# Kernel optimization log

Measured on AMD Instinct MI355X. Metric: run time of the kernel, lower is better.

The kernel has to match this reference:

```python
import jax, jax.numpy as jnp
import numpy as np

D_MODEL = 1024
NUM_HEADS = 16
DK = D_MODEL // NUM_HEADS


def setup_inputs() -> dict:
    key = jax.random.key(0)
    ks = jax.random.split(key, 12)
    B, S, D = 2, 2048, D_MODEL
    s = 1.0 / np.sqrt(D)
    inp = {
        "Q": jax.random.normal(ks[0], (B, S, D), jnp.float32),
        "K": jax.random.normal(ks[1], (B, S, D), jnp.float32),
        "V": jax.random.normal(ks[2], (B, S, D), jnp.float32),
        "Wq": jax.random.uniform(ks[3], (D, D), jnp.float32, -s, s),
        "bq": jax.random.uniform(ks[4], (D,), jnp.float32, -s, s),
        "Wk": jax.random.uniform(ks[5], (D, D), jnp.float32, -s, s),
        "bk": jax.random.uniform(ks[6], (D,), jnp.float32, -s, s),
        "Wv": jax.random.uniform(ks[7], (D, D), jnp.float32, -s, s),
        "bv": jax.random.uniform(ks[8], (D,), jnp.float32, -s, s),
        "Wo": jax.random.uniform(ks[9], (D, D), jnp.float32, -s, s),
        "bo": jax.random.uniform(ks[10], (D,), jnp.float32, -s, s),
    }
    return inp


def reference(Q, K, V, Wq, bq, Wk, bk, Wv, bv, Wo, bo):
    B, S, D = Q.shape
    H, dk = NUM_HEADS, DK
    # projections (torch Linear: x @ W.T + b), split heads -> [B,H,S,dk]
    q = (Q @ Wq.T + bq).reshape(B, S, H, dk).transpose(0, 2, 1, 3)
    k = (K @ Wk.T + bk).reshape(B, S, H, dk).transpose(0, 2, 1, 3)
    v = (V @ Wv.T + bv).reshape(B, S, H, dk).transpose(0, 2, 1, 3)
    scores = jnp.einsum("bhqd,bhkd->bhqk", q, k) / jnp.sqrt(jnp.asarray(dk, q.dtype))
    attn = jax.nn.softmax(scores, axis=-1)
    out = jnp.einsum("bhqk,bhkd->bhqd", attn, v)  # [B,H,S,dk]
    out = out.transpose(0, 2, 1, 3).reshape(B, S, D)
    return out @ Wo.T + bo
```

## Files before the change

### kernel.cpp

```cpp
#include <hip/hip_runtime.h>
#include <stdint.h>


#define AS1 __attribute__((address_space(1)))
#define AS3 __attribute__((address_space(3)))

typedef unsigned short u16;
typedef short s16x8 __attribute__((ext_vector_type(8)));
typedef float f32x4 __attribute__((ext_vector_type(4)));
typedef float f32x16 __attribute__((ext_vector_type(16)));
typedef u16   u16x4 __attribute__((ext_vector_type(4)));

#if defined(__has_builtin)
#if __has_builtin(__builtin_amdgcn_exp2f)
#define EXP2F(x) __builtin_amdgcn_exp2f(x)
#else
#define EXP2F(x) exp2f(x)
#endif
#else
#define EXP2F(x) exp2f(x)
#endif

__device__ __forceinline__ u16 f2b(float f) {
  union { float f; uint32_t u; } v;
  v.f = f;
  uint32_t r = (v.u + 0x7fffu + ((v.u >> 16) & 1u)) >> 16;
  return (u16)r;
}

__device__ __forceinline__ uint32_t cvtpk(float lo, float hi) {
  uint32_t r;
  asm("v_cvt_pk_bf16_f32 %0, %1, %2" : "=v"(r) : "v"(lo), "v"(hi));
  return r;
}

__device__ __forceinline__ float max3f(float a, float b, float c) {
  float r;
  asm("v_max3_f32 %0, %1, %2, %3" : "=v"(r) : "v"(a), "v"(b), "v"(c));
  return r;
}

__device__ __forceinline__ f32x4 mfma16(s16x8 a, s16x8 b, f32x4 c) {
  return __builtin_amdgcn_mfma_f32_16x16x32_bf16(a, b, c, 0, 0, 0);
}

__device__ __forceinline__ f32x16 mfma32(s16x8 a, s16x8 b, f32x16 c) {
  return __builtin_amdgcn_mfma_f32_32x32x16_bf16(a, b, c, 0, 0, 0);
}

__device__ __forceinline__ s16x8 ld_g16(const u16* p) {
  return *reinterpret_cast<const s16x8*>(p);
}

__device__ __forceinline__ void stage16(const u16* g, u16* lds_base) {
  __builtin_amdgcn_global_load_lds((const AS1 unsigned int*)g,
                                   (AS3 unsigned int*)lds_base, 16, 0, 0);
}

struct CvtArgs {
  const float* src[7];
  u16* dst[7];
  int cum[8];
};

__global__ __launch_bounds__(256) void cvt_all(CvtArgs a) {
  const int bx = blockIdx.x;
  int seg = 0;
#pragma unroll
  for (int i = 1; i < 7; ++i) seg += (bx >= a.cum[i]) ? 1 : 0;
  const int off = (bx - a.cum[seg]) * 256 + threadIdx.x;
  float4 f = reinterpret_cast<const float4*>(a.src[seg])[off];
  union { u16 u[4]; uint64_t q; } o;
  o.u[0] = f2b(f.x); o.u[1] = f2b(f.y); o.u[2] = f2b(f.z); o.u[3] = f2b(f.w);
  reinterpret_cast<uint64_t*>(a.dst[seg])[off] = o.q;
}

template <int MODE>
__global__ __launch_bounds__(256) void gemm_bt(const u16* __restrict__ Abase,
                                               const u16* __restrict__ Wbase,
                                               const float* __restrict__ bias0,
                                               const float* __restrict__ bias1,
                                               const float* __restrict__ bias2,
                                               u16* __restrict__ outb,
                                               u16* __restrict__ vtout,
                                               float* __restrict__ outf) {
  __shared__ u16 As[2][128 * 64];
  __shared__ u16 Bs[2][128 * 64];
  const int tid = threadIdx.x;
  const int lane = tid & 63;
  const int w = tid >> 6;
  const int wr = w >> 1, wc = w & 1;

  const int bid = blockIdx.y * 8 + blockIdx.x;
  const int sw = (bid & 7) * 32 + (bid >> 3);
  const int n0 = (sw & 7) * 128;
  const int m0 = (sw >> 3) * 128;
  const int z = (MODE == 0) ? blockIdx.z : 0;
  const float QSC = 0.18033688011112042f;

  const u16* A = Abase + (size_t)z * (4096u * 1024u);
  const u16* W = Wbase + (size_t)z * (1024u * 1024u);
  const float* bias = (MODE == 0) ? (z == 0 ? bias0 : (z == 1 ? bias1 : bias2)) : bias0;
  u16* ob = (MODE == 0) ? (outb + (size_t)z * (4096u * 1024u)) : nullptr;

  const int l15 = lane & 15, l4 = lane >> 4;

  const int sr = lane >> 3;
  const int sx = lane & 7;
  const u16* gA[4];
  const u16* gB[4];
#pragma unroll
  for (int j = 0; j < 4; ++j) {
    const int row = w * 32 + j * 8 + sr;
    const int lc = ((sx ^ (row & 7)) << 3);
    gA[j] = A + (size_t)(m0 + row) * 1024 + lc;
    gB[j] = W + (size_t)(n0 + row) * 1024 + lc;
  }

  f32x4 acc[4][4];
#pragma unroll
  for (int i = 0; i < 4; ++i)
#pragma unroll
    for (int j = 0; j < 4; ++j) acc[i][j] = {0.f, 0.f, 0.f, 0.f};

#pragma unroll
  for (int j = 0; j < 4; ++j) {
    stage16(gA[j], &As[0][(w * 32 + j * 8) * 64]);
    stage16(gB[j], &Bs[0][(w * 32 + j * 8) * 64]);
  }
  __syncthreads();

#pragma unroll 2
  for (int t = 0; t < 16; ++t) {
    const int cur = t & 1;
    if (t + 1 < 16) {
      const int kt = (t + 1) * 64;
#pragma unroll
      for (int j = 0; j < 4; ++j) {
        stage16(gA[j] + kt, &As[cur ^ 1][(w * 32 + j * 8) * 64]);
        stage16(gB[j] + kt, &Bs[cur ^ 1][(w * 32 + j * 8) * 64]);
      }
    }
#pragma unroll
    for (int ks = 0; ks < 2; ++ks) {
      s16x8 af[4], bf[4];
#pragma unroll
      for (int mi = 0; mi < 4; ++mi) {
        const int row = wr * 64 + mi * 16 + l15;
        const int sc_ = (((ks << 2) | l4) ^ (l15 & 7)) << 3;
        af[mi] = *(const s16x8*)&As[cur][row * 64 + sc_];
      }
#pragma unroll
      for (int ni = 0; ni < 4; ++ni) {
        const int row = wc * 64 + ni * 16 + l15;
        const int sc_ = (((ks << 2) | l4) ^ (l15 & 7)) << 3;
        bf[ni] = *(const s16x8*)&Bs[cur][row * 64 + sc_];
      }
      __builtin_amdgcn_s_setprio(1);
#pragma unroll
      for (int mi = 0; mi < 4; ++mi)
#pragma unroll
        for (int ni = 0; ni < 4; ++ni)
          acc[mi][ni] = mfma16(af[mi], bf[ni], acc[mi][ni]);
      __builtin_amdgcn_s_setprio(0);
    }
    __syncthreads();
  }

#pragma unroll
  for (int ni = 0; ni < 4; ++ni) {
    const int col = n0 + wc * 64 + ni * 16 + l15;
    const float bv = bias[col];
#pragma unroll
    for (int mi = 0; mi < 4; ++mi) {
      const int row0 = m0 + wr * 64 + mi * 16 + l4 * 4;
      if (MODE == 0 && z == 2) {
        const int b = row0 >> 11, s0 = row0 & 2047;
        const int pos0 = (s0 & ~15) | ((s0 & 4) << 1) | ((s0 & 8) >> 1);
        const int h = col >> 6, d = col & 63;
        u16x4 pk = {f2b(acc[mi][ni][0] + bv), f2b(acc[mi][ni][1] + bv),
                    f2b(acc[mi][ni][2] + bv), f2b(acc[mi][ni][3] + bv)};
        *(u16x4*)&vtout[((size_t)(b * 16 + h) * 64 + d) * 2048 + pos0] = pk;
      } else {
#pragma unroll
        for (int r = 0; r < 4; ++r) {
          float val = acc[mi][ni][r] + bv;
          const int row = row0 + r;
          if (MODE == 0) {
            if (z == 0) val *= QSC;
            const int b = row >> 11, s = row & 2047;
            const int h = col >> 6, d = col & 63;
            ob[((size_t)(b * 16 + h) * 2048 + s) * 64 + d] = f2b(val);
          } else {
            outf[(size_t)row * 1024 + col] = val;
          }
        }
      }
    }
  }
}

__global__ __launch_bounds__(512, 2) void fattn(const u16* __restrict__ qp,
                                                const u16* __restrict__ kp,
                                                const u16* __restrict__ vt,
                                                u16* __restrict__ ao) {
  __shared__ u16 Kt[2][4096];
  __shared__ u16 Vt[2][4096];

  const int lane = threadIdx.x & 63;
  const int w = threadIdx.x >> 6;
  const int bh = blockIdx.y;
  const int b = bh >> 4, h = bh & 15;
  const int q0 = blockIdx.x * 256 + w * 32;
  const u16* qb = qp + (size_t)bh * (2048 * 64);
  const u16* kb = kp + (size_t)bh * (2048 * 64);
  const u16* vb = vt + (size_t)bh * (64 * 2048);
  const int l31 = lane & 31, hl = lane >> 5;
  const int x7 = l31 & 7;
  const float THR = 8.0f;

  const int srow = (w << 3) + (lane >> 3);
  const int c0 = (((lane & 7) ^ (srow & 7)) << 3);

  s16x8 qa[4];
#pragma unroll
  for (int kc = 0; kc < 4; ++kc)
    qa[kc] = ld_g16(qb + (size_t)(q0 + l31) * 64 + kc * 16 + hl * 8);

  f32x16 o[2];
  float lsum = 0.f;
  float mrun = 0.f;
#pragma unroll
  for (int r = 0; r < 16; ++r) { o[0][r] = 0.f; o[1][r] = 0.f; }

  stage16(kb + (size_t)srow * 64 + c0, &Kt[0][w * 512]);
  stage16(vb + (size_t)srow * 2048 + c0, &Vt[0][w * 512]);
  __syncthreads();

#pragma unroll 2
  for (int t = 0; t < 32; ++t) {
    const int cur = t & 1;
    if (t + 1 < 32) {
      const int kk = (t + 1) << 6;
      stage16(kb + (size_t)(kk + srow) * 64 + c0, &Kt[cur ^ 1][w * 512]);
      stage16(vb + (size_t)srow * 2048 + kk + c0, &Vt[cur ^ 1][w * 512]);
    }

    f32x16 sc[2];
#pragma unroll
    for (int r = 0; r < 16; ++r) { sc[0][r] = -mrun; sc[1][r] = -mrun; }
#pragma unroll
    for (int nk = 0; nk < 2; ++nk) {
      s16x8 kf[4];
#pragma unroll
      for (int kc = 0; kc < 4; ++kc)
        kf[kc] = *(const s16x8*)&Kt[cur][(nk * 32 + l31) * 64 +
                                         ((((kc << 1) | hl) ^ x7) << 3)];
      __builtin_amdgcn_s_setprio(1);
#pragma unroll
      for (int kc = 0; kc < 4; ++kc)
        sc[nk] = mfma32(kf[kc], qa[kc], sc[nk]);
      __builtin_amdgcn_s_setprio(0);
    }

    float m = -1e30f;
#pragma unroll
    for (int nk = 0; nk < 2; ++nk)
#pragma unroll
      for (int r = 0; r < 16; r += 2)
        m = max3f(m, sc[nk][r], sc[nk][r + 1]);
    m = fmaxf(m, __shfl_xor(m, 32));

    if (__any(m > THR)) {
      const float d = fmaxf(m, 0.f);
      mrun += d;
      const float alpha = EXP2F(-d);
      lsum *= alpha;
#pragma unroll
      for (int r = 0; r < 16; ++r) { sc[0][r] -= d; sc[1][r] -= d; }
#pragma unroll
      for (int r = 0; r < 16; ++r) {
        float ar = __shfl(alpha, (r & 3) + 8 * (r >> 2) + 4 * hl);
        o[0][r] *= ar; o[1][r] *= ar;
      }
    }

#pragma unroll
    for (int nk = 0; nk < 2; ++nk) {
      float p[16];
#pragma unroll
      for (int r = 0; r < 16; ++r) p[r] = EXP2F(sc[nk][r]);
#pragma unroll
      for (int r = 0; r < 16; ++r) lsum += p[r];
#pragma unroll
      for (int kc = 0; kc < 2; ++kc) {
        union { uint32_t d[4]; s16x8 v; } pa;
        pa.d[0] = cvtpk(p[kc * 8 + 0], p[kc * 8 + 1]);
        pa.d[1] = cvtpk(p[kc * 8 + 2], p[kc * 8 + 3]);
        pa.d[2] = cvtpk(p[kc * 8 + 4], p[kc * 8 + 5]);
        pa.d[3] = cvtpk(p[kc * 8 + 6], p[kc * 8 + 7]);
        const int chunk = nk * 4 + kc * 2 + hl;
#pragma unroll
        for (int dt = 0; dt < 2; ++dt) {
          s16x8 vf = *(const s16x8*)&Vt[cur][(dt * 32 + l31) * 64 +
                                             ((chunk ^ x7) << 3)];
          __builtin_amdgcn_s_setprio(1);
          o[dt] = mfma32(pa.v, vf, o[dt]);
          __builtin_amdgcn_s_setprio(0);
        }
      }
    }

    __syncthreads();
  }

  lsum += __shfl_xor(lsum, 32);
#pragma unroll
  for (int r = 0; r < 16; ++r) {
    const int qreg = (r & 3) + 8 * (r >> 2) + 4 * hl;
    const float inv = 1.0f / __shfl(lsum, qreg);
    const int row = b * 2048 + q0 + qreg;
#pragma unroll
    for (int dt = 0; dt < 2; ++dt)
      ao[(size_t)row * 1024 + h * 64 + dt * 32 + l31] = f2b(o[dt][r] * inv);
  }
}

extern "C" void kernel_launch(void* const* d_in, const int* in_sizes, int n_in,
                              void* d_out, int out_size, void* d_ws, size_t ws_size,
                              hipStream_t stream) {
  const float* Q  = (const float*)d_in[0];
  const float* K  = (const float*)d_in[1];
  const float* V  = (const float*)d_in[2];
  const float* Wq = (const float*)d_in[3];
  const float* bq = (const float*)d_in[4];
  const float* Wk = (const float*)d_in[5];
  const float* bk = (const float*)d_in[6];
  const float* Wv = (const float*)d_in[7];
  const float* bv = (const float*)d_in[8];
  const float* Wo = (const float*)d_in[9];
  const float* bo = (const float*)d_in[10];
  float* out = (float*)d_out;

  const size_t NI = (size_t)4096 * 1024;
  const size_t NW = (size_t)1024 * 1024;
  u16* XB  = (u16*)d_ws;
  u16* WB  = XB + 3 * NI;
  u16* QKV = WB + 4 * NW;
  u16* VT  = QKV + 3 * NI;
  u16* AO  = VT + NI;

  CvtArgs ca;
  ca.src[0] = Q;  ca.dst[0] = XB;
  ca.src[1] = K;  ca.dst[1] = XB + NI;
  ca.src[2] = V;  ca.dst[2] = XB + 2 * NI;
  ca.src[3] = Wq; ca.dst[3] = WB;
  ca.src[4] = Wk; ca.dst[4] = WB + NW;
  ca.src[5] = Wv; ca.dst[5] = WB + 2 * NW;
  ca.src[6] = Wo; ca.dst[6] = WB + 3 * NW;
  ca.cum[0] = 0;     ca.cum[1] = 4096;  ca.cum[2] = 8192;  ca.cum[3] = 12288;
  ca.cum[4] = 13312; ca.cum[5] = 14336; ca.cum[6] = 15360; ca.cum[7] = 16384;
  cvt_all<<<dim3(16384), 256, 0, stream>>>(ca);

  gemm_bt<0><<<dim3(8, 32, 3), 256, 0, stream>>>(XB, WB, bq, bk, bv, QKV, VT, nullptr);
  fattn<<<dim3(8, 32), 512, 0, stream>>>(QKV, QKV + NI, VT, AO);
  gemm_bt<1><<<dim3(8, 32, 1), 256, 0, stream>>>(AO, WB + 3 * NW, bo, nullptr, nullptr,
                                                 nullptr, nullptr, out);
}
```

Baseline: 128.0 us.

## Software-pipeline attention: overlap next tile's QK^T with softmax/PV using triple-buffered LDS

Restructures the flash-attention kernel so the QK^T MFMAs for the next key tile are issued while the current tile's softmax and PV run. It adds a third LDS buffer rotated between staging, QK and PV roles, with a lagged running-max correction. Blocks shrink from 8 waves to 4 waves and 128 queries, and the grid doubles to keep the same coverage. This is meant to hide MFMA and LDS latency behind exp work, at the cost of more registers for the two score sets and more LDS per block.

Measured after the change: 133.2 us. +4.1%, slower.

```diff
diff --git a/kernel.cpp b/kernel.cpp
--- a/kernel.cpp
+++ b/kernel.cpp
@@ -200,18 +200,20 @@
   }
 }
 
-__global__ __launch_bounds__(512, 2) void fattn(const u16* __restrict__ qp,
+__global__ __launch_bounds__(256, 2) void fattn(const u16* __restrict__ qp,
                                                 const u16* __restrict__ kp,
                                                 const u16* __restrict__ vt,
                                                 u16* __restrict__ ao) {
-  __shared__ u16 Kt[2][4096];
-  __shared__ u16 Vt[2][4096];
+  __shared__ u16 Kt[3][4096];
+  __shared__ u16 Vt[3][4096];
+  u16* Ksh = &Kt[0][0];
+  u16* Vsh = &Vt[0][0];
 
   const int lane = threadIdx.x & 63;
   const int w = threadIdx.x >> 6;
   const int bh = blockIdx.y;
   const int b = bh >> 4, h = bh & 15;
-  const int q0 = blockIdx.x * 256 + w * 32;
+  const int q0 = blockIdx.x * 128 + w * 32;
   const u16* qb = qp + (size_t)bh * (2048 * 64);
   const u16* kb = kp + (size_t)bh * (2048 * 64);
   const u16* vb = vt + (size_t)bh * (64 * 2048);
@@ -219,100 +221,131 @@
   const int x7 = l31 & 7;
   const float THR = 8.0f;
 
-  const int srow = (w << 3) + (lane >> 3);
-  const int c0 = (((lane & 7) ^ (srow & 7)) << 3);
+  const int srow = (w << 4) + (lane >> 3);
+  const int c0 = (((lane & 7) ^ (lane >> 3)) << 3);
+
+#define STAGE(kk, bo)                                                          \
+  do {                                                                         \
+    stage16(kb + (size_t)((kk) + srow) * 64 + c0, Ksh + (bo) + w * 1024);      \
+    stage16(kb + (size_t)((kk) + srow + 8) * 64 + c0, Ksh + (bo) + w * 1024 + 512); \
+    stage16(vb + (size_t)srow * 2048 + (kk) + c0, Vsh + (bo) + w * 1024);      \
+    stage16(vb + (size_t)(srow + 8) * 2048 + (kk) + c0, Vsh + (bo) + w * 1024 + 512); \
+  } while (0)
 
   s16x8 qa[4];
 #pragma unroll
   for (int kc = 0; kc < 4; ++kc)
     qa[kc] = ld_g16(qb + (size_t)(q0 + l31) * 64 + kc * 16 + hl * 8);
 
-  f32x16 o[2];
+  f32x16 o0, o1;
+  f32x16 scA0, scA1, scB0, scB1;
   float lsum = 0.f;
   float mrun = 0.f;
-#pragma unroll
-  for (int r = 0; r < 16; ++r) { o[0][r] = 0.f; o[1][r] = 0.f; }
-
-  stage16(kb + (size_t)srow * 64 + c0, &Kt[0][w * 512]);
-  stage16(vb + (size_t)srow * 2048 + c0, &Vt[0][w * 512]);
+  float mbA = 0.f, mbB = 0.f;
+#pragma unroll
+  for (int r = 0; r < 16; ++r) { o0[r] = 0.f; o1[r] = 0.f; }
+
+#define QKT(N0, N1, MBN, BO)                                                   \
+  do {                                                                         \
+    MBN = mrun;                                                                \
+    const float ini_ = -mrun;                                                  \
+    _Pragma("unroll") for (int r = 0; r < 16; ++r) { N0[r] = ini_; N1[r] = ini_; } \
+    s16x8 kf0_[4], kf1_[4];                                                    \
+    _Pragma("unroll") for (int kc = 0; kc < 4; ++kc) {                         \
+      kf0_[kc] = *(const s16x8*)&Ksh[(BO) + (0 * 32 + l31) * 64 +              \
+                                     ((((kc << 1) | hl) ^ x7) << 3)];          \
+      kf1_[kc] = *(const s16x8*)&Ksh[(BO) + (1 * 32 + l31) * 64 +              \
+                                     ((((kc << 1) | hl) ^ x7) << 3)];          \
+    }                                                                          \
+    __builtin_amdgcn_s_setprio(1);                                             \
+    _Pragma("unroll") for (int kc = 0; kc < 4; ++kc) N0 = mfma32(kf0_[kc], qa[kc], N0); \
+    _Pragma("unroll") for (int kc = 0; kc < 4; ++kc) N1 = mfma32(kf1_[kc], qa[kc], N1); \
+    __builtin_amdgcn_s_setprio(0);                                             \
+  } while (0)
+
+#define SMPV(S0, S1, MB, BO)                                                   \
+  do {                                                                         \
+    float x1 = max3f(S0[0], S0[1], S0[2]);                                     \
+    float x2 = max3f(S0[3], S0[4], S0[5]);                                     \
+    float x3 = max3f(S0[6], S0[7], S0[8]);                                     \
+    float x4 = max3f(S0[9], S0[10], S0[11]);                                   \
+    float x5 = max3f(S0[12], S0[13], S0[14]);                                  \
+    float x6 = max3f(S0[15], S1[0], S1[1]);                                    \
+    float x7_ = max3f(S1[2], S1[3], S1[4]);                                    \
+    float x8 = max3f(S1[5], S1[6], S1[7]);                                     \
+    float x9 = max3f(S1[8], S1[9], S1[10]);                                    \
+    float xa = max3f(S1[11], S1[12], S1[13]);                                  \
+    float xb = max3f(S1[14], S1[15], x1);                                      \
+    float xc = max3f(x2, x3, x4);                                              \
+    float xd = max3f(x5, x6, x7_);                                             \
+    float xe = max3f(x8, x9, xa);                                              \
+    float mrel = fmaxf(max3f(xb, xc, xd), xe);                                 \
+    mrel = fmaxf(mrel, __shfl_xor(mrel, 32));                                  \
+    float base_ = MB - mrun;                                                   \
+    if (__any(mrel + base_ > THR)) {                  \
+      float d_ = fmaxf(mrel + base_, 0.f);                                     \
+      mrun += d_; base_ -= d_;                                                 \
+      float al_ = EXP2F(-d_);                                                  \
+      lsum *= al_;                                                             \
+      _Pragma("unroll") for (int r = 0; r < 16; ++r) {                         \
+        float ar_ = __shfl(al_, (r & 3) + 8 * (r >> 2) + 4 * hl);              \
+        o0[r] *= ar_; o1[r] *= ar_;                                            \
+      }                                                                        \
+    }                                                                          \
+    if (__any(base_ != 0.f)) {                      \
+      _Pragma("unroll") for (int r = 0; r < 16; ++r) { S0[r] += base_; S1[r] += base_; } \
+    }                                                                          \
+    float p0_[16], p1_[16];                                                    \
+    _Pragma("unroll") for (int r = 0; r < 16; ++r) p0_[r] = EXP2F(S0[r]);      \
+    _Pragma("unroll") for (int r = 0; r < 16; ++r) p1_[r] = EXP2F(S1[r]);      \
+    _Pragma("unroll") for (int r = 0; r < 16; ++r) lsum += p0_[r] + p1_[r];    \
+    _Pragma("unroll") for (int nk = 0; nk < 2; ++nk) {                         \
+      float* pp_ = nk ? p1_ : p0_;                                             \
+      _Pragma("unroll") for (int kc = 0; kc < 2; ++kc) {                       \
+        union { uint32_t d[4]; s16x8 v; } pa_;                                 \
+        pa_.d[0] = cvtpk(pp_[kc * 8 + 0], pp_[kc * 8 + 1]);                    \
+        pa_.d[1] = cvtpk(pp_[kc * 8 + 2], pp_[kc * 8 + 3]);                    \
+        pa_.d[2] = cvtpk(pp_[kc * 8 + 4], pp_[kc * 8 + 5]);                    \
+        pa_.d[3] = cvtpk(pp_[kc * 8 + 6], pp_[kc * 8 + 7]);                    \
+        const int chunk_ = nk * 4 + kc * 2 + hl;                               \
+        s16x8 vf0_ = *(const s16x8*)&Vsh[(BO) + (0 * 32 + l31) * 64 +          \
+                                         ((chunk_ ^ x7) << 3)];                \
+        s16x8 vf1_ = *(const s16x8*)&Vsh[(BO) + (1 * 32 + l31) * 64 +          \
+                                         ((chunk_ ^ x7) << 3)];                \
+        __builtin_amdgcn_s_setprio(1);                                         \
+        o0 = mfma32(pa_.v, vf0_, o0);                                          \
+        o1 = mfma32(pa_.v, vf1_, o1);                                          \
+        __builtin_amdgcn_s_setprio(0);                                         \
+      }                                                                        \
+    }                                                                          \
+  } while (0)
+
+#define ROT()                                                                  \
+  do { const int t_ = b_pv; b_pv = b_qk; b_qk = b_st; b_st = t_; } while (0)
+
+  int b_pv = 0, b_qk = 4096, b_st = 8192;
+
+  STAGE(0, 0);
   __syncthreads();
-
-#pragma unroll 2
-  for (int t = 0; t < 32; ++t) {
-    const int cur = t & 1;
-    if (t + 1 < 32) {
-      const int kk = (t + 1) << 6;
-      stage16(kb + (size_t)(kk + srow) * 64 + c0, &Kt[cur ^ 1][w * 512]);
-      stage16(vb + (size_t)srow * 2048 + kk + c0, &Vt[cur ^ 1][w * 512]);
-    }
-
-    f32x16 sc[2];
-#pragma unroll
-    for (int r = 0; r < 16; ++r) { sc[0][r] = -mrun; sc[1][r] = -mrun; }
-#pragma unroll
-    for (int nk = 0; nk < 2; ++nk) {
-      s16x8 kf[4];
-#pragma unroll
-      for (int kc = 0; kc < 4; ++kc)
-        kf[kc] = *(const s16x8*)&Kt[cur][(nk * 32 + l31) * 64 +
-                                         ((((kc << 1) | hl) ^ x7) << 3)];
-      __builtin_amdgcn_s_setprio(1);
-#pragma unroll
-      for (int kc = 0; kc < 4; ++kc)
-        sc[nk] = mfma32(kf[kc], qa[kc], sc[nk]);
-      __builtin_amdgcn_s_setprio(0);
-    }
-
-    float m = -1e30f;
-#pragma unroll
-    for (int nk = 0; nk < 2; ++nk)
-#pragma unroll
-      for (int r = 0; r < 16; r += 2)
-        m = max3f(m, sc[nk][r], sc[nk][r + 1]);
-    m = fmaxf(m, __shfl_xor(m, 32));
-
-    if (__any(m > THR)) {
-      const float d = fmaxf(m, 0.f);
-      mrun += d;
-      const float alpha = EXP2F(-d);
-      lsum *= alpha;
-#pragma unroll
-      for (int r = 0; r < 16; ++r) { sc[0][r] -= d; sc[1][r] -= d; }
-#pragma unroll
-      for (int r = 0; r < 16; ++r) {
-        float ar = __shfl(alpha, (r & 3) + 8 * (r >> 2) + 4 * hl);
-        o[0][r] *= ar; o[1][r] *= ar;
-      }
-    }
-
-#pragma unroll
-    for (int nk = 0; nk < 2; ++nk) {
-      float p[16];
-#pragma unroll
-      for (int r = 0; r < 16; ++r) p[r] = EXP2F(sc[nk][r]);
-#pragma unroll
-      for (int r = 0; r < 16; ++r) lsum += p[r];
-#pragma unroll
-      for (int kc = 0; kc < 2; ++kc) {
-        union { uint32_t d[4]; s16x8 v; } pa;
-        pa.d[0] = cvtpk(p[kc * 8 + 0], p[kc * 8 + 1]);
-        pa.d[1] = cvtpk(p[kc * 8 + 2], p[kc * 8 + 3]);
-        pa.d[2] = cvtpk(p[kc * 8 + 4], p[kc * 8 + 5]);
-        pa.d[3] = cvtpk(p[kc * 8 + 6], p[kc * 8 + 7]);
-        const int chunk = nk * 4 + kc * 2 + hl;
-#pragma unroll
-        for (int dt = 0; dt < 2; ++dt) {
-          s16x8 vf = *(const s16x8*)&Vt[cur][(dt * 32 + l31) * 64 +
-                                             ((chunk ^ x7) << 3)];
-          __builtin_amdgcn_s_setprio(1);
-          o[dt] = mfma32(pa.v, vf, o[dt]);
-          __builtin_amdgcn_s_setprio(0);
-        }
-      }
-    }
-
+  STAGE(64, 4096);
+  QKT(scA0, scA1, mbA, 0);
+  __syncthreads();
+
+  for (int it = 0; it < 15; ++it) {
+    STAGE(it * 128 + 128, b_st);
+    QKT(scB0, scB1, mbB, b_qk);
+    SMPV(scA0, scA1, mbA, b_pv);
     __syncthreads();
-  }
+    ROT();
+    STAGE(it * 128 + 192, b_st);
+    QKT(scA0, scA1, mbA, b_qk);
+    SMPV(scB0, scB1, mbB, b_pv);
+    __syncthreads();
+    ROT();
+  }
+  QKT(scB0, scB1, mbB, b_qk);
+  SMPV(scA0, scA1, mbA, b_pv);
+  SMPV(scB0, scB1, mbB, b_qk);
 
   lsum += __shfl_xor(lsum, 32);
 #pragma unroll
@@ -320,10 +353,13 @@
     const int qreg = (r & 3) + 8 * (r >> 2) + 4 * hl;
     const float inv = 1.0f / __shfl(lsum, qreg);
     const int row = b * 2048 + q0 + qreg;
-#pragma unroll
-    for (int dt = 0; dt < 2; ++dt)
-      ao[(size_t)row * 1024 + h * 64 + dt * 32 + l31] = f2b(o[dt][r] * inv);
-  }
+    ao[(size_t)row * 1024 + h * 64 + 0 * 32 + l31] = f2b(o0[r] * inv);
+    ao[(size_t)row * 1024 + h * 64 + 1 * 32 + l31] = f2b(o1[r] * inv);
+  }
+#undef STAGE
+#undef QKT
+#undef SMPV
+#undef ROT
 }
 
 extern "C" void kernel_launch(void* const* d_in, const int* in_sizes, int n_in,
@@ -363,7 +399,7 @@
   cvt_all<<<dim3(16384), 256, 0, stream>>>(ca);
 
   gemm_bt<0><<<dim3(8, 32, 3), 256, 0, stream>>>(XB, WB, bq, bk, bv, QKV, VT, nullptr);
-  fattn<<<dim3(8, 32), 512, 0, stream>>>(QKV, QKV + NI, VT, AO);
+  fattn<<<dim3(16, 32), 256, 0, stream>>>(QKV, QKV + NI, VT, AO);
   gemm_bt<1><<<dim3(8, 32, 1), 256, 0, stream>>>(AO, WB + 3 * NW, bo, nullptr, nullptr,
                                                  nullptr, nullptr, out);
 }
```

## Process 64 query rows per wave in flash attention with 256-thread blocks

Applied to the files above, without the earlier changes.

Each wave now handles two 32-row query tiles instead of one, so every K and V fragment read from LDS feeds two MFMAs. Blocks shrink from 512 to 256 threads, and each thread stages twice as many K/V rows, keeping the same 256-query tile per block. The goal is to cut LDS read traffic per MFMA and raise instruction-level parallelism. The cost is doubled accumulator and score registers, which may lower occupancy or cause spills, and fewer waves per block to hide latency.

Measured after the change: 138.6 us. +8.2%, slower.

```diff
diff --git a/kernel.cpp b/kernel.cpp
--- a/kernel.cpp
+++ b/kernel.cpp
@@ -200,10 +200,10 @@
   }
 }
 
-__global__ __launch_bounds__(512, 2) void fattn(const u16* __restrict__ qp,
-                                                const u16* __restrict__ kp,
-                                                const u16* __restrict__ vt,
-                                                u16* __restrict__ ao) {
+__global__ __launch_bounds__(256) void fattn(const u16* __restrict__ qp,
+                                             const u16* __restrict__ kp,
+                                             const u16* __restrict__ vt,
+                                             u16* __restrict__ ao) {
   __shared__ u16 Kt[2][4096];
   __shared__ u16 Vt[2][4096];
 
@@ -211,7 +211,7 @@
   const int w = threadIdx.x >> 6;
   const int bh = blockIdx.y;
   const int b = bh >> 4, h = bh & 15;
-  const int q0 = blockIdx.x * 256 + w * 32;
+  const int q0 = blockIdx.x * 256 + w * 64;
   const u16* qb = qp + (size_t)bh * (2048 * 64);
   const u16* kb = kp + (size_t)bh * (2048 * 64);
   const u16* vb = vt + (size_t)bh * (64 * 2048);
@@ -219,22 +219,26 @@
   const int x7 = l31 & 7;
   const float THR = 8.0f;
 
-  const int srow = (w << 3) + (lane >> 3);
+  const int srow = (w << 4) + (lane >> 3);
   const int c0 = (((lane & 7) ^ (srow & 7)) << 3);
 
-  s16x8 qa[4];
-#pragma unroll
-  for (int kc = 0; kc < 4; ++kc)
-    qa[kc] = ld_g16(qb + (size_t)(q0 + l31) * 64 + kc * 16 + hl * 8);
-
-  f32x16 o[2];
-  float lsum = 0.f;
-  float mrun = 0.f;
-#pragma unroll
-  for (int r = 0; r < 16; ++r) { o[0][r] = 0.f; o[1][r] = 0.f; }
-
-  stage16(kb + (size_t)srow * 64 + c0, &Kt[0][w * 512]);
-  stage16(vb + (size_t)srow * 2048 + c0, &Vt[0][w * 512]);
+  s16x8 qa0[4], qa1[4];
+#pragma unroll
+  for (int kc = 0; kc < 4; ++kc) {
+    qa0[kc] = ld_g16(qb + (size_t)(q0 + l31) * 64 + kc * 16 + hl * 8);
+    qa1[kc] = ld_g16(qb + (size_t)(q0 + 32 + l31) * 64 + kc * 16 + hl * 8);
+  }
+
+  f32x16 o00, o01, o10, o11;
+  float lsum0 = 0.f, lsum1 = 0.f;
+  float mrun0 = 0.f, mrun1 = 0.f;
+#pragma unroll
+  for (int r = 0; r < 16; ++r) { o00[r] = 0.f; o01[r] = 0.f; o10[r] = 0.f; o11[r] = 0.f; }
+
+  stage16(kb + (size_t)srow * 64 + c0, &Kt[0][w * 1024]);
+  stage16(kb + (size_t)(srow + 8) * 64 + c0, &Kt[0][w * 1024 + 512]);
+  stage16(vb + (size_t)srow * 2048 + c0, &Vt[0][w * 1024]);
+  stage16(vb + (size_t)(srow + 8) * 2048 + c0, &Vt[0][w * 1024 + 512]);
   __syncthreads();
 
 #pragma unroll 2
@@ -242,13 +246,18 @@
     const int cur = t & 1;
     if (t + 1 < 32) {
       const int kk = (t + 1) << 6;
-      stage16(kb + (size_t)(kk + srow) * 64 + c0, &Kt[cur ^ 1][w * 512]);
-      stage16(vb + (size_t)srow * 2048 + kk + c0, &Vt[cur ^ 1][w * 512]);
-    }
-
-    f32x16 sc[2];
-#pragma unroll
-    for (int r = 0; r < 16; ++r) { sc[0][r] = -mrun; sc[1][r] = -mrun; }
+      stage16(kb + (size_t)(kk + srow) * 64 + c0, &Kt[cur ^ 1][w * 1024]);
+      stage16(kb + (size_t)(kk + srow + 8) * 64 + c0, &Kt[cur ^ 1][w * 1024 + 512]);
+      stage16(vb + (size_t)srow * 2048 + kk + c0, &Vt[cur ^ 1][w * 1024]);
+      stage16(vb + (size_t)(srow + 8) * 2048 + kk + c0, &Vt[cur ^ 1][w * 1024 + 512]);
+    }
+
+    f32x16 s00, s01, s10, s11;
+#pragma unroll
+    for (int r = 0; r < 16; ++r) {
+      s00[r] = -mrun0; s01[r] = -mrun0;
+      s10[r] = -mrun1; s11[r] = -mrun1;
+    }
 #pragma unroll
     for (int nk = 0; nk < 2; ++nk) {
       s16x8 kf[4];
@@ -257,72 +266,135 @@
         kf[kc] = *(const s16x8*)&Kt[cur][(nk * 32 + l31) * 64 +
                                          ((((kc << 1) | hl) ^ x7) << 3)];
       __builtin_amdgcn_s_setprio(1);
-#pragma unroll
-      for (int kc = 0; kc < 4; ++kc)
-        sc[nk] = mfma32(kf[kc], qa[kc], sc[nk]);
+      if (nk == 0) {
+#pragma unroll
+        for (int kc = 0; kc < 4; ++kc) s00 = mfma32(kf[kc], qa0[kc], s00);
+#pragma unroll
+        for (int kc = 0; kc < 4; ++kc) s10 = mfma32(kf[kc], qa1[kc], s10);
+      } else {
+#pragma unroll
+        for (int kc = 0; kc < 4; ++kc) s01 = mfma32(kf[kc], qa0[kc], s01);
+#pragma unroll
+        for (int kc = 0; kc < 4; ++kc) s11 = mfma32(kf[kc], qa1[kc], s11);
+      }
       __builtin_amdgcn_s_setprio(0);
     }
 
-    float m = -1e30f;
-#pragma unroll
-    for (int nk = 0; nk < 2; ++nk)
-#pragma unroll
-      for (int r = 0; r < 16; r += 2)
-        m = max3f(m, sc[nk][r], sc[nk][r + 1]);
-    m = fmaxf(m, __shfl_xor(m, 32));
-
-    if (__any(m > THR)) {
-      const float d = fmaxf(m, 0.f);
-      mrun += d;
-      const float alpha = EXP2F(-d);
-      lsum *= alpha;
-#pragma unroll
-      for (int r = 0; r < 16; ++r) { sc[0][r] -= d; sc[1][r] -= d; }
+    float m0 = fmaxf(s00[0], s00[1]);
+#pragma unroll
+    for (int r = 2; r < 16; r += 2) m0 = max3f(m0, s00[r], s00[r + 1]);
+#pragma unroll
+    for (int r = 0; r < 16; r += 2) m0 = max3f(m0, s01[r], s01[r + 1]);
+    m0 = fmaxf(m0, __shfl_xor(m0, 32));
+    float m1 = fmaxf(s10[0], s10[1]);
+#pragma unroll
+    for (int r = 2; r < 16; r += 2) m1 = max3f(m1, s10[r], s10[r + 1]);
+#pragma unroll
+    for (int r = 0; r < 16; r += 2) m1 = max3f(m1, s11[r], s11[r + 1]);
+    m1 = fmaxf(m1, __shfl_xor(m1, 32));
+
+    if (__any(fmaxf(m0, m1) > THR)) {
+      const float d0 = fmaxf(m0, 0.f);
+      mrun0 += d0;
+      const float al0 = EXP2F(-d0);
+      lsum0 *= al0;
 #pragma unroll
       for (int r = 0; r < 16; ++r) {
-        float ar = __shfl(alpha, (r & 3) + 8 * (r >> 2) + 4 * hl);
-        o[0][r] *= ar; o[1][r] *= ar;
-      }
-    }
-
-#pragma unroll
-    for (int nk = 0; nk < 2; ++nk) {
-      float p[16];
-#pragma unroll
-      for (int r = 0; r < 16; ++r) p[r] = EXP2F(sc[nk][r]);
-#pragma unroll
-      for (int r = 0; r < 16; ++r) lsum += p[r];
+        float ar = __shfl(al0, (r & 3) + 8 * (r >> 2) + 4 * hl);
+        o00[r] *= ar; o01[r] *= ar;
+      }
+#pragma unroll
+      for (int r = 0; r < 16; ++r) { s00[r] -= d0; s01[r] -= d0; }
+      const float d1 = fmaxf(m1, 0.f);
+      mrun1 += d1;
+      const float al1 = EXP2F(-d1);
+      lsum1 *= al1;
+#pragma unroll
+      for (int r = 0; r < 16; ++r) {
+        float ar = __shfl(al1, (r & 3) + 8 * (r >> 2) + 4 * hl);
+        o10[r] *= ar; o11[r] *= ar;
+      }
+#pragma unroll
+      for (int r = 0; r < 16; ++r) { s10[r] -= d1; s11[r] -= d1; }
+    }
+
+    {
+      float p0[16], p1[16];
+#pragma unroll
+      for (int r = 0; r < 16; ++r) p0[r] = EXP2F(s00[r]);
+#pragma unroll
+      for (int r = 0; r < 16; ++r) p1[r] = EXP2F(s10[r]);
+#pragma unroll
+      for (int r = 0; r < 16; ++r) { lsum0 += p0[r]; lsum1 += p1[r]; }
 #pragma unroll
       for (int kc = 0; kc < 2; ++kc) {
-        union { uint32_t d[4]; s16x8 v; } pa;
-        pa.d[0] = cvtpk(p[kc * 8 + 0], p[kc * 8 + 1]);
-        pa.d[1] = cvtpk(p[kc * 8 + 2], p[kc * 8 + 3]);
-        pa.d[2] = cvtpk(p[kc * 8 + 4], p[kc * 8 + 5]);
-        pa.d[3] = cvtpk(p[kc * 8 + 6], p[kc * 8 + 7]);
-        const int chunk = nk * 4 + kc * 2 + hl;
-#pragma unroll
-        for (int dt = 0; dt < 2; ++dt) {
-          s16x8 vf = *(const s16x8*)&Vt[cur][(dt * 32 + l31) * 64 +
-                                             ((chunk ^ x7) << 3)];
-          __builtin_amdgcn_s_setprio(1);
-          o[dt] = mfma32(pa.v, vf, o[dt]);
-          __builtin_amdgcn_s_setprio(0);
-        }
+        union { uint32_t d[4]; s16x8 v; } pa0, pa1;
+        pa0.d[0] = cvtpk(p0[kc * 8 + 0], p0[kc * 8 + 1]);
+        pa0.d[1] = cvtpk(p0[kc * 8 + 2], p0[kc * 8 + 3]);
+        pa0.d[2] = cvtpk(p0[kc * 8 + 4], p0[kc * 8 + 5]);
+        pa0.d[3] = cvtpk(p0[kc * 8 + 6], p0[kc * 8 + 7]);
+        pa1.d[0] = cvtpk(p1[kc * 8 + 0], p1[kc * 8 + 1]);
+        pa1.d[1] = cvtpk(p1[kc * 8 + 2], p1[kc * 8 + 3]);
+        pa1.d[2] = cvtpk(p1[kc * 8 + 4], p1[kc * 8 + 5]);
+        pa1.d[3] = cvtpk(p1[kc * 8 + 6], p1[kc * 8 + 7]);
+        const int chunk = 0 * 4 + kc * 2 + hl;
+        s16x8 vf0 = *(const s16x8*)&Vt[cur][(0 * 32 + l31) * 64 + ((chunk ^ x7) << 3)];
+        s16x8 vf1 = *(const s16x8*)&Vt[cur][(1 * 32 + l31) * 64 + ((chunk ^ x7) << 3)];
+        __builtin_amdgcn_s_setprio(1);
+        o00 = mfma32(pa0.v, vf0, o00);
+        o10 = mfma32(pa1.v, vf0, o10);
+        o01 = mfma32(pa0.v, vf1, o01);
+        o11 = mfma32(pa1.v, vf1, o11);
+        __builtin_amdgcn_s_setprio(0);
+      }
+    }
+    {
+      float p0[16], p1[16];
+#pragma unroll
+      for (int r = 0; r < 16; ++r) p0[r] = EXP2F(s01[r]);
+#pragma unroll
+      for (int r = 0; r < 16; ++r) p1[r] = EXP2F(s11[r]);
+#pragma unroll
+      for (int r = 0; r < 16; ++r) { lsum0 += p0[r]; lsum1 += p1[r]; }
+#pragma unroll
+      for (int kc = 0; kc < 2; ++kc) {
+        union { uint32_t d[4]; s16x8 v; } pa0, pa1;
+        pa0.d[0] = cvtpk(p0[kc * 8 + 0], p0[kc * 8 + 1]);
+        pa0.d[1] = cvtpk(p0[kc * 8 + 2], p0[kc * 8 + 3]);
+        pa0.d[2] = cvtpk(p0[kc * 8 + 4], p0[kc * 8 + 5]);
+        pa0.d[3] = cvtpk(p0[kc * 8 + 6], p0[kc * 8 + 7]);
+        pa1.d[0] = cvtpk(p1[kc * 8 + 0], p1[kc * 8 + 1]);
+        pa1.d[1] = cvtpk(p1[kc * 8 + 2], p1[kc * 8 + 3]);
+        pa1.d[2] = cvtpk(p1[kc * 8 + 4], p1[kc * 8 + 5]);
+        pa1.d[3] = cvtpk(p1[kc * 8 + 6], p1[kc * 8 + 7]);
+        const int chunk = 1 * 4 + kc * 2 + hl;
+        s16x8 vf0 = *(const s16x8*)&Vt[cur][(0 * 32 + l31) * 64 + ((chunk ^ x7) << 3)];
+        s16x8 vf1 = *(const s16x8*)&Vt[cur][(1 * 32 + l31) * 64 + ((chunk ^ x7) << 3)];
+        __builtin_amdgcn_s_setprio(1);
+        o00 = mfma32(pa0.v, vf0, o00);
+        o10 = mfma32(pa1.v, vf0, o10);
+        o01 = mfma32(pa0.v, vf1, o01);
+        o11 = mfma32(pa1.v, vf1, o11);
+        __builtin_amdgcn_s_setprio(0);
       }
     }
 
     __syncthreads();
   }
 
-  lsum += __shfl_xor(lsum, 32);
+  lsum0 += __shfl_xor(lsum0, 32);
+  lsum1 += __shfl_xor(lsum1, 32);
 #pragma unroll
   for (int r = 0; r < 16; ++r) {
     const int qreg = (r & 3) + 8 * (r >> 2) + 4 * hl;
-    const float inv = 1.0f / __shfl(lsum, qreg);
-    const int row = b * 2048 + q0 + qreg;
-#pragma unroll
-    for (int dt = 0; dt < 2; ++dt)
-      ao[(size_t)row * 1024 + h * 64 + dt * 32 + l31] = f2b(o[dt][r] * inv);
+    const float inv0 = 1.0f / __shfl(lsum0, qreg);
+    const float inv1 = 1.0f / __shfl(lsum1, qreg);
+    const int row0 = b * 2048 + q0 + qreg;
+    const int row1 = row0 + 32;
+    ao[(size_t)row0 * 1024 + h * 64 + l31]      = f2b(o00[r] * inv0);
+    ao[(size_t)row0 * 1024 + h * 64 + 32 + l31] = f2b(o01[r] * inv0);
+    ao[(size_t)row1 * 1024 + h * 64 + l31]      = f2b(o10[r] * inv1);
+    ao[(size_t)row1 * 1024 + h * 64 + 32 + l31] = f2b(o11[r] * inv1);
   }
 }
 
@@ -363,7 +435,7 @@
   cvt_all<<<dim3(16384), 256, 0, stream>>>(ca);
 
   gemm_bt<0><<<dim3(8, 32, 3), 256, 0, stream>>>(XB, WB, bq, bk, bv, QKV, VT, nullptr);
-  fattn<<<dim3(8, 32), 512, 0, stream>>>(QKV, QKV + NI, VT, AO);
+  fattn<<<dim3(8, 32), 256, 0, stream>>>(QKV, QKV + NI, VT, AO);
   gemm_bt<1><<<dim3(8, 32, 1), 256, 0, stream>>>(AO, WB + 3 * NW, bo, nullptr, nullptr,
                                                  nullptr, nullptr, out);
 }
```

## Fuse fp32-to-bf16 activation conversion into the QKV projection GEMM loads

Applied to the files above, without the earlier changes.

Drops the separate conversion of Q/K/V inputs to bf16 and instead has the QKV GEMM load fp32 tiles into registers, convert them, and write bf16 into LDS for the next stage. This removes a full write-and-reread of the bf16 activation copies in global memory and shrinks the conversion kernel to weights only. In exchange the A operand loses the async global-to-LDS path, adding register pressure and exposed load latency inside the GEMM loop.

New measurement: 121.4 us. 1.05x faster.

```diff
diff --git a/kernel.cpp b/kernel.cpp
--- a/kernel.cpp
+++ b/kernel.cpp
@@ -58,16 +58,16 @@
 }
 
 struct CvtArgs {
-  const float* src[7];
-  u16* dst[7];
-  int cum[8];
+  const float* src[4];
+  u16* dst[4];
+  int cum[5];
 };
 
 __global__ __launch_bounds__(256) void cvt_all(CvtArgs a) {
   const int bx = blockIdx.x;
   int seg = 0;
 #pragma unroll
-  for (int i = 1; i < 7; ++i) seg += (bx >= a.cum[i]) ? 1 : 0;
+  for (int i = 1; i < 4; ++i) seg += (bx >= a.cum[i]) ? 1 : 0;
   const int off = (bx - a.cum[seg]) * 256 + threadIdx.x;
   float4 f = reinterpret_cast<const float4*>(a.src[seg])[off];
   union { u16 u[4]; uint64_t q; } o;
@@ -76,7 +76,10 @@
 }
 
 template <int MODE>
-__global__ __launch_bounds__(256) void gemm_bt(const u16* __restrict__ Abase,
+__global__ __launch_bounds__(256) void gemm_bt(const float* __restrict__ Aq,
+                                               const float* __restrict__ Ak,
+                                               const float* __restrict__ Av,
+                                               const u16* __restrict__ Abf,
                                                const u16* __restrict__ Wbase,
                                                const float* __restrict__ bias0,
                                                const float* __restrict__ bias1,
@@ -98,7 +101,7 @@
   const int z = (MODE == 0) ? blockIdx.z : 0;
   const float QSC = 0.18033688011112042f;
 
-  const u16* A = Abase + (size_t)z * (4096u * 1024u);
+  const float* Af = (MODE == 0) ? (z == 0 ? Aq : (z == 1 ? Ak : Av)) : nullptr;
   const u16* W = Wbase + (size_t)z * (1024u * 1024u);
   const float* bias = (MODE == 0) ? (z == 0 ? bias0 : (z == 1 ? bias1 : bias2)) : bias0;
   u16* ob = (MODE == 0) ? (outb + (size_t)z * (4096u * 1024u)) : nullptr;
@@ -107,13 +110,15 @@
 
   const int sr = lane >> 3;
   const int sx = lane & 7;
-  const u16* gA[4];
+  const float* gAf[4];
+  const u16* gAb[4];
   const u16* gB[4];
 #pragma unroll
   for (int j = 0; j < 4; ++j) {
     const int row = w * 32 + j * 8 + sr;
     const int lc = ((sx ^ (row & 7)) << 3);
-    gA[j] = A + (size_t)(m0 + row) * 1024 + lc;
+    if (MODE == 0) gAf[j] = Af + (size_t)(m0 + row) * 1024 + lc;
+    else           gAb[j] = Abf + (size_t)(m0 + row) * 1024 + lc;
     gB[j] = W + (size_t)(n0 + row) * 1024 + lc;
   }
 
@@ -125,7 +130,16 @@
 
 #pragma unroll
   for (int j = 0; j < 4; ++j) {
-    stage16(gA[j], &As[0][(w * 32 + j * 8) * 64]);
+    if (MODE == 0) {
+      float4 b0 = *(const float4*)gAf[j];
+      float4 b1 = *(const float4*)(gAf[j] + 4);
+      union { uint32_t d[4]; s16x8 v; } cv;
+      cv.d[0] = cvtpk(b0.x, b0.y); cv.d[1] = cvtpk(b0.z, b0.w);
+      cv.d[2] = cvtpk(b1.x, b1.y); cv.d[3] = cvtpk(b1.z, b1.w);
+      *(s16x8*)&As[0][(w * 32 + j * 8) * 64 + lane * 8] = cv.v;
+    } else {
+      stage16(gAb[j], &As[0][(w * 32 + j * 8) * 64]);
+    }
     stage16(gB[j], &Bs[0][(w * 32 + j * 8) * 64]);
   }
   __syncthreads();
@@ -133,13 +147,24 @@
 #pragma unroll 2
   for (int t = 0; t < 16; ++t) {
     const int cur = t & 1;
-    if (t + 1 < 16) {
+    float4 a0[4], a1[4];
+    const bool more = (t + 1 < 16);
+    if (more) {
       const int kt = (t + 1) * 64;
-#pragma unroll
-      for (int j = 0; j < 4; ++j) {
-        stage16(gA[j] + kt, &As[cur ^ 1][(w * 32 + j * 8) * 64]);
+      if (MODE == 0) {
+#pragma unroll
+        for (int j = 0; j < 4; ++j) {
+          a0[j] = *(const float4*)(gAf[j] + kt);
+          a1[j] = *(const float4*)(gAf[j] + kt + 4);
+        }
+      } else {
+#pragma unroll
+        for (int j = 0; j < 4; ++j)
+          stage16(gAb[j] + kt, &As[cur ^ 1][(w * 32 + j * 8) * 64]);
+      }
+#pragma unroll
+      for (int j = 0; j < 4; ++j)
         stage16(gB[j] + kt, &Bs[cur ^ 1][(w * 32 + j * 8) * 64]);
-      }
     }
 #pragma unroll
     for (int ks = 0; ks < 2; ++ks) {
@@ -163,6 +188,15 @@
         for (int ni = 0; ni < 4; ++ni)
           acc[mi][ni] = mfma16(af[mi], bf[ni], acc[mi][ni]);
       __builtin_amdgcn_s_setprio(0);
+    }
+    if (more && MODE == 0) {
+#pragma unroll
+      for (int j = 0; j < 4; ++j) {
+        union { uint32_t d[4]; s16x8 v; } cv;
+        cv.d[0] = cvtpk(a0[j].x, a0[j].y); cv.d[1] = cvtpk(a0[j].z, a0[j].w);
+        cv.d[2] = cvtpk(a1[j].x, a1[j].y); cv.d[3] = cvtpk(a1[j].z, a1[j].w);
+        *(s16x8*)&As[cur ^ 1][(w * 32 + j * 8) * 64 + lane * 8] = cv.v;
+      }
     }
     __syncthreads();
   }
@@ -344,26 +378,23 @@
 
   const size_t NI = (size_t)4096 * 1024;
   const size_t NW = (size_t)1024 * 1024;
-  u16* XB  = (u16*)d_ws;
-  u16* WB  = XB + 3 * NI;
+  u16* WB  = (u16*)d_ws;
   u16* QKV = WB + 4 * NW;
   u16* VT  = QKV + 3 * NI;
   u16* AO  = VT + NI;
 
   CvtArgs ca;
-  ca.src[0] = Q;  ca.dst[0] = XB;
-  ca.src[1] = K;  ca.dst[1] = XB + NI;
-  ca.src[2] = V;  ca.dst[2] = XB + 2 * NI;
-  ca.src[3] = Wq; ca.dst[3] = WB;
-  ca.src[4] = Wk; ca.dst[4] = WB + NW;
-  ca.src[5] = Wv; ca.dst[5] = WB + 2 * NW;
-  ca.src[6] = Wo; ca.dst[6] = WB + 3 * NW;
-  ca.cum[0] = 0;     ca.cum[1] = 4096;  ca.cum[2] = 8192;  ca.cum[3] = 12288;
-  ca.cum[4] = 13312; ca.cum[5] = 14336; ca.cum[6] = 15360; ca.cum[7] = 16384;
-  cvt_all<<<dim3(16384), 256, 0, stream>>>(ca);
-
-  gemm_bt<0><<<dim3(8, 32, 3), 256, 0, stream>>>(XB, WB, bq, bk, bv, QKV, VT, nullptr);
+  ca.src[0] = Wq; ca.dst[0] = WB;
+  ca.src[1] = Wk; ca.dst[1] = WB + NW;
+  ca.src[2] = Wv; ca.dst[2] = WB + 2 * NW;
+  ca.src[3] = Wo; ca.dst[3] = WB + 3 * NW;
+  ca.cum[0] = 0; ca.cum[1] = 1024; ca.cum[2] = 2048; ca.cum[3] = 3072; ca.cum[4] = 4096;
+  cvt_all<<<dim3(4096), 256, 0, stream>>>(ca);
+
+  gemm_bt<0><<<dim3(8, 32, 3), 256, 0, stream>>>(Q, K, V, nullptr, WB, bq, bk, bv,
+                                                 QKV, VT, nullptr);
   fattn<<<dim3(8, 32), 512, 0, stream>>>(QKV, QKV + NI, VT, AO);
-  gemm_bt<1><<<dim3(8, 32, 1), 256, 0, stream>>>(AO, WB + 3 * NW, bo, nullptr, nullptr,
+  gemm_bt<1><<<dim3(8, 32, 1), 256, 0, stream>>>(nullptr, nullptr, nullptr, AO,
+                                                 WB + 3 * NW, bo, nullptr, nullptr,
                                                  nullptr, nullptr, out);
 }
```
